# Kernel tuning notes

Hardware: AMD Instinct MI355X
Metric: run time of the kernel (lower is better)

Reference implementation:

```python
import jax, jax.numpy as jnp
import numpy as np

H_DIM = 256
N_HEADS = 8
HALF = H_DIM // 2

def _lin(x, W, b):
    # torch nn.Linear: y = x @ W.T + b
    y = x @ W.T
    return y + b if b is not None else y

def setup_inputs() -> dict:
    key = jax.random.key(0)
    ks = jax.random.split(key, 16)
    s = 0.02
    d = {
        'x': jax.random.normal(ks[0], (16, H_DIM, 32, 32), jnp.float32),
        'q1_w': jax.random.normal(ks[1], (HALF, HALF), jnp.float32) * s,
        'q1_b': jnp.zeros((HALF,), jnp.float32),
        'q2_w': jax.random.normal(ks[2], (HALF, HALF), jnp.float32) * s,
        'q2_b': jnp.zeros((HALF,), jnp.float32),
        'k1_w': jax.random.normal(ks[3], (HALF, HALF), jnp.float32) * s,
        'k1_b': jnp.zeros((HALF,), jnp.float32),
        'k2_w': jax.random.normal(ks[4], (HALF, HALF), jnp.float32) * s,
        'k2_b': jnp.zeros((HALF,), jnp.float32),
        'v1_w': jax.random.normal(ks[5], (HALF, HALF), jnp.float32) * s,
        'v1_b': jnp.zeros((HALF,), jnp.float32),
        'v2_w': jax.random.normal(ks[6], (HALF, HALF), jnp.float32) * s,
        'v2_b': jnp.zeros((HALF,), jnp.float32),
        'proj1_w': jax.random.normal(ks[7], (HALF, HALF), jnp.float32) * s,
        'proj1_b': jnp.zeros((HALF,), jnp.float32),
        'proj2_w': jax.random.normal(ks[8], (HALF, HALF), jnp.float32) * s,
        'proj2_b': jnp.zeros((HALF,), jnp.float32),
        'logit_scale': jnp.log(10.0 * jnp.ones((N_HEADS, 1, 1), jnp.float32)),
        'mlp_w1': jax.random.normal(ks[9], (128, 2), jnp.float32) * s,
        'mlp_b1': jnp.zeros((128,), jnp.float32),
        'mlp_w2': jax.random.normal(ks[10], (N_HEADS, 128), jnp.float32) * s,
    }
    return d

def _rel_pos_index(h, w):
    # static (numpy) relative position index, shape [N, N]
    ch, cw = np.meshgrid(np.arange(h), np.arange(w), indexing='ij')
    coords = np.stack([ch.reshape(-1), cw.reshape(-1)])  # [2, N]
    rel = coords[:, :, None] - coords[:, None, :]         # [2, N, N]
    rel = rel.transpose(1, 2, 0)
    rel[:, :, 0] += h - 1
    rel[:, :, 1] += w - 1
    return rel[:, :, 0] * (2 * w - 1) + rel[:, :, 1]

def _forward(x, q1_w, q1_b, q2_w, q2_b, k1_w, k1_b, k2_w, k2_b,
             v1_w, v1_b, v2_w, v2_b, proj1_w, proj1_b, proj2_w, proj2_b,
             logit_scale, mlp_w1, mlp_b1, mlp_w2):
    b, c, h, w = x.shape
    N = h * w
    nh = N_HEADS
    hd = c // nh
    x3 = jnp.transpose(x, (0, 2, 3, 1)).reshape(b, N, c)
    x0, x1 = x3[..., :c // 2], x3[..., c // 2:]

    def qkv(W0, b0, W1, b1):
        t = jnp.concatenate([x0 + _lin(x0, W0, b0), x1 + _lin(x1, W1, b1)], axis=-1)
        return t.reshape(b, N, nh, hd).transpose(0, 2, 1, 3)  # [b, nh, N, hd]

    q = qkv(q1_w, q1_b, q2_w, q2_b)
    k = qkv(k1_w, k1_b, k2_w, k2_b)
    v = qkv(v1_w, v1_b, v2_w, v2_b)

    eps = 1e-12
    qn = q / jnp.maximum(jnp.linalg.norm(q, axis=-1, keepdims=True), eps)
    kn = k / jnp.maximum(jnp.linalg.norm(k, axis=-1, keepdims=True), eps)
    attn = jnp.einsum('bhnd,bhmd->bhnm', qn, kn)  # cosine similarity
    scale = jnp.exp(jnp.minimum(logit_scale, jnp.log(1.0 / 0.01)))  # [nh,1,1]
    attn = attn * scale[None]

    # continuous relative-position bias (CPB) table via small MLP
    rch = jnp.arange(-(h - 1), h, dtype=jnp.float32) / (h - 1 + 1e-8)
    rcw = jnp.arange(-(w - 1), w, dtype=jnp.float32) / (w - 1 + 1e-8)
    gh, gw = jnp.meshgrid(rch, rcw, indexing='ij')
    tab = jnp.stack([gh, gw], axis=-1) * 3.2               # [2h-1, 2w-1, 2]
    tab = jnp.sign(tab) * (1.0 - jnp.exp(-jnp.abs(tab)))
    tab = jax.nn.relu(_lin(tab, mlp_w1, mlp_b1))
    tab = _lin(tab, mlp_w2, None).reshape(-1, nh)          # [(2h-1)(2w-1), nh]

    idx = jnp.asarray(_rel_pos_index(h, w))                # [N, N]
    bias = tab[idx.reshape(-1)].reshape(N, N, nh).transpose(2, 0, 1)
    bias = 16.0 * jax.nn.sigmoid(bias)
    attn = attn + bias[None]

    attn = jax.nn.softmax(attn, axis=-1)
    out = jnp.einsum('bhnm,bhmd->bhnd', attn, v).transpose(0, 2, 1, 3).reshape(b, N, c)
    o0, o1 = out[..., :c // 2], out[..., c // 2:]
    out = jnp.concatenate([_lin(o0, proj1_w, proj1_b), _lin(o1, proj2_w, proj2_b)], axis=-1)
    return out.reshape(b, h, w, c).transpose(0, 3, 1, 2)

def reference(x, q1_w, q1_b, q2_w, q2_b, k1_w, k1_b, k2_w, k2_b,
              v1_w, v1_b, v2_w, v2_b, proj1_w, proj1_b, proj2_w, proj2_b,
              logit_scale, mlp_w1, mlp_b1, mlp_w2):
    return _forward(x, q1_w, q1_b, q2_w, q2_b, k1_w, k1_b, k2_w, k2_b,
                    v1_w, v1_b, v2_w, v2_b, proj1_w, proj1_b, proj2_w, proj2_b,
                    logit_scale, mlp_w1, mlp_b1, mlp_w2)
```

## Files before the change

kernel.cpp:

```cpp
#include <hip/hip_runtime.h>
#include <cmath>


typedef _Float16 half_t;
typedef __attribute__((ext_vector_type(4))) _Float16 half4;
typedef __attribute__((ext_vector_type(8))) _Float16 half8;
typedef __attribute__((ext_vector_type(4))) float float4v;

static __device__ __forceinline__ float4v mfma16(half8 a, half8 b, float4v c) {
  return __builtin_amdgcn_mfma_f32_16x16x32_f16(a, b, c, 0, 0, 0);
}

struct PtrArr8 { const float* p[8]; };

__global__ __launch_bounds__(256) void prep_w(PtrArr8 wsrc, PtrArr8 bsrc,
                                              half_t* __restrict__ wf,
                                              float* __restrict__ bws) {
  int y = blockIdx.y;
  const float* src = nullptr;
  const float* bs = nullptr;
#pragma unroll
  for (int i = 0; i < 8; i++)
    if (i == y) { src = wsrc.p[i]; bs = bsrc.p[i]; }
  int flat = (blockIdx.x * 256 + threadIdx.x) * 4;
  float4 w = *(const float4*)(src + flat);
  int j = flat >> 7, k = flat & 127;
  if (y < 6) {
    if (k == j)     w.x += 1.0f;
    if (k + 1 == j) w.y += 1.0f;
    if (k + 2 == j) w.z += 1.0f;
    if (k + 3 == j) w.w += 1.0f;
  }
  half4 h;
  h[0] = (half_t)w.x;
  h[1] = (half_t)w.y;
  h[2] = (half_t)w.z;
  h[3] = (half_t)w.w;
  int ng = j >> 4, l = j & 15, ks = k >> 5, quad = (k >> 3) & 3, o8 = k & 7;
  *(half4*)(wf + y * 16384 + ((ng * 4 + ks) * 64 + quad * 16 + l) * 8 + o8) =
      h;
  if (blockIdx.x == 0 && threadIdx.x < 128)
    bws[y * 128 + threadIdx.x] = bs[threadIdx.x];
}

__global__ __launch_bounds__(256) void bias_mlp(const float* __restrict__ w1,
                                                const float* __restrict__ b1,
                                                const float* __restrict__ w2,
                                                const float* __restrict__ ls,
                                                float* __restrict__ tabh2) {
  __shared__ float sw1[256];
  __shared__ float sb1[128];
  __shared__ float sw2[1024];
  int t = threadIdx.x;
  sw1[t] = w1[t];
  if (t < 128) sb1[t] = b1[t];
  for (int i = t; i < 1024; i += 256) sw2[i] = w2[i];
  __syncthreads();
  int p = blockIdx.x * 256 + t;
  if (p >= 3969) return;
  int ph = p / 63, pw = p % 63;
  float t0 = (float)(ph - 31) * (3.2f / 31.0f);
  float t1 = (float)(pw - 31) * (3.2f / 31.0f);
  t0 = copysignf(1.0f - __expf(-fabsf(t0)), t0);
  t1 = copysignf(1.0f - __expf(-fabsf(t1)), t1);
  float acc[8];
#pragma unroll
  for (int hh = 0; hh < 8; hh++) acc[hh] = 0.0f;
  for (int j = 0; j < 128; j++) {
    float hj = fmaxf(0.0f, t0 * sw1[2 * j] + t1 * sw1[2 * j + 1] + sb1[j]);
#pragma unroll
    for (int hh = 0; hh < 8; hh++) acc[hh] += hj * sw2[hh * 128 + j];
  }
  const float L2E = 1.44269504f;
#pragma unroll
  for (int hh = 0; hh < 8; hh++) {
    float scale = __expf(fminf(ls[hh], 4.6051702f));
    float c14 = 14.0f - (scale + 16.0f) * L2E;
    float bias = 16.0f / (1.0f + __expf(-acc[hh]));
    tabh2[hh * 3969 + p] = bias * L2E + c14;
  }
}

__global__ __launch_bounds__(256, 4) void qkv_mfma(
    const float* __restrict__ x, const half_t* __restrict__ wfrag,
    const float* __restrict__ lscale, const float* __restrict__ bws,
    half_t* __restrict__ qf, half_t* __restrict__ kf,
    half_t* __restrict__ vf) {
  __shared__ half_t tbuf[4608];
  int t = threadIdx.x;
  int lane = t & 63, wv = t >> 6, l = lane & 15, quad = lane >> 4;
  int rw = wv & 1, cw = wv >> 1;
  int hf = blockIdx.y;
  int m0 = blockIdx.x * 32;
  int b = m0 >> 10, n0 = m0 & 1023;

  half8 afr[4];
  {
    const float* xb =
        x + ((size_t)b * 256 + hf * 128) * 1024 + n0 + rw * 16 + l;
#pragma unroll
    for (int ks = 0; ks < 4; ks++) {
      half8 a;
#pragma unroll
      for (int j = 0; j < 8; j++)
        a[j] = (half_t)xb[(size_t)(ks * 32 + quad * 8 + j) * 1024];
      afr[ks] = a;
    }
  }

  for (int op = 0; op < 3; op++) {
    int combo = op * 2 + hf;
    const half_t* wfb = wfrag + combo * 16384;
    float4v acc[4];
#pragma unroll
    for (int ngl = 0; ngl < 4; ngl++) {
      int ng = cw * 4 + ngl;
      float4v c = {0.f, 0.f, 0.f, 0.f};
#pragma unroll
      for (int ks = 0; ks < 4; ks++) {
        half8 bfrag =
            *(const half8*)(wfb + ((ng * 4 + ks) * 64 + lane) * 8);
        c = mfma16(afr[ks], bfrag, c);
      }
      acc[ngl] = c;
    }
#pragma unroll
    for (int ngl = 0; ngl < 4; ngl++) {
      float bb = bws[combo * 128 + (cw * 4 + ngl) * 16 + l];
#pragma unroll
      for (int r2 = 0; r2 < 4; r2++) acc[ngl][r2] += bb;
    }
    if (op < 2) {
#pragma unroll
      for (int hgl = 0; hgl < 2; hgl++) {
        float sc = 1.0f;
        if (op == 0)
          sc = __expf(fminf(lscale[hf * 4 + cw * 2 + hgl], 4.6051702f)) *
               1.44269504f;
#pragma unroll
        for (int r2 = 0; r2 < 4; r2++) {
          float ss = acc[2 * hgl][r2] * acc[2 * hgl][r2] +
                     acc[2 * hgl + 1][r2] * acc[2 * hgl + 1][r2];
          ss += __shfl_xor(ss, 1, 64);
          ss += __shfl_xor(ss, 2, 64);
          ss += __shfl_xor(ss, 4, 64);
          ss += __shfl_xor(ss, 8, 64);
          float rn = sc / fmaxf(sqrtf(ss), 1e-12f);
          acc[2 * hgl][r2] *= rn;
          acc[2 * hgl + 1][r2] *= rn;
        }
      }
#pragma unroll
      for (int ngl = 0; ngl < 4; ngl++)
#pragma unroll
        for (int r2 = 0; r2 < 4; r2++)
          tbuf[(rw * 16 + quad * 4 + r2) * 136 + (cw * 4 + ngl) * 16 + l] =
              (half_t)acc[ngl][r2];
      __syncthreads();
      half_t* dst = (op == 0) ? qf : kf;
#pragma unroll
      for (int i = 0; i < 2; i++) {
        int idx = t + 256 * i;
        int row = idx >> 4, colc = (idx & 15) * 8;
        half8 vv = *(const half8*)(tbuf + row * 136 + colc);
        int head = hf * 4 + (colc >> 5), d = colc & 31;
        *(half8*)(dst + (((size_t)b * 8 + head) * 1024 + n0 + row) * 32 + d) =
            vv;
      }
      __syncthreads();
    } else {
#pragma unroll
      for (int ngl = 0; ngl < 4; ngl++) {
        int col = (cw * 4 + ngl) * 16 + l;
        half4 hv;
#pragma unroll
        for (int r2 = 0; r2 < 4; r2++) hv[r2] = (half_t)acc[ngl][r2];
        *(half4*)(tbuf + col * 36 + rw * 16 + quad * 4) = hv;
      }
      __syncthreads();
#pragma unroll
      for (int i = 0; i < 8; i++) {
        int idx = t + 256 * i;
        int col = idx >> 4, rp = idx & 15;
        unsigned int val = *(const unsigned int*)(tbuf + col * 36 + rp * 2);
        int head = hf * 4 + (col >> 5);
        int d = col & 31;
        *(unsigned int*)((char*)vf +
                         (((((size_t)b * 8 + head) * 32 + d) * 1024) + n0 +
                          rp * 2) * 2) = val;
      }
    }
  }
}

__global__ __launch_bounds__(256) void attn_mfma(
    const half_t* __restrict__ qf, const half_t* __restrict__ kf,
    const half_t* __restrict__ vf, const float* __restrict__ tabh2,
    half_t* __restrict__ ao) {
  __shared__ float sb2[35 * 63];
  __shared__ half_t pa[4 * 16 * 80];

  int id = blockIdx.x;
  int qo = id >> 7;
  int bh = id & 127;
  int h = bh & 7, b = bh >> 3;
  int t = threadIdx.x;
  int lane = t & 63, wv = t >> 6, l = lane & 15, quad = lane >> 4;
  size_t bhs = (size_t)b * 8 + h;
  const half_t* kbase = kf + bhs * 1024 * 32;
  const half_t* vbase = vf + bhs * 32 * 1024;

  for (int i = t; i < 2205; i += 256)
    sb2[i] = tabh2[h * 3969 + qo * 252 + i];

  int row0 = qo * 128 + wv * 32;
  half8 qfr[2];
#pragma unroll
  for (int s = 0; s < 2; s++)
    qfr[s] = *(const half8*)(qf + (bhs * 1024 + row0 + s * 16 + l) * 32 +
                             quad * 8);

  float4v o0[2], o1[2];
  float run_l[2];
#pragma unroll
  for (int s = 0; s < 2; s++) {
    o0[s] = (float4v){0.f, 0.f, 0.f, 0.f};
    o1[s] = (float4v){0.f, 0.f, 0.f, 0.f};
    run_l[s] = 0.0f;
  }
  half_t* paw = pa + wv * 16 * 80;
  __syncthreads();

#pragma unroll 2
  for (int kt = 0; kt < 16; kt++) {
    half8 kfr[4], v0fr[2], v1fr[2];
#pragma unroll
    for (int nt = 0; nt < 4; nt++)
      kfr[nt] =
          *(const half8*)(kbase + (kt * 64 + nt * 16 + l) * 32 + quad * 8);
#pragma unroll
    for (int ks = 0; ks < 2; ks++) {
      v0fr[ks] = *(const half8*)(vbase + l * 1024 + kt * 64 + ks * 32 +
                                 quad * 8);
      v1fr[ks] = *(const half8*)(vbase + (16 + l) * 1024 + kt * 64 + ks * 32 +
                                 quad * 8);
    }
#pragma unroll
    for (int s = 0; s < 2; s++) {
      float4v sres[4];
#pragma unroll
      for (int nt = 0; nt < 4; nt++) {
        int base = (wv - 2 * kt - (nt >> 1) + 31) * 63 + s * 16 + l + 31 -
                   (nt & 1) * 16 - quad * 4;
        float4v c;
        c[0] = sb2[base];
        c[1] = sb2[base - 1];
        c[2] = sb2[base - 2];
        c[3] = sb2[base - 3];
        sres[nt] = mfma16(kfr[nt], qfr[s], c);
      }
#pragma unroll
      for (int nt = 0; nt < 4; nt++) {
        half4 ph;
#pragma unroll
        for (int r2 = 0; r2 < 4; r2++) {
          float p = exp2f(sres[nt][r2]);
          run_l[s] += p;
          ph[r2] = (half_t)p;
        }
        *(half4*)(paw + l * 80 + nt * 16 + quad * 4) = ph;
      }
#pragma unroll
      for (int ks = 0; ks < 2; ks++) {
        half8 pfr = *(const half8*)(paw + l * 80 + ks * 32 + quad * 8);
        o0[s] = mfma16(pfr, v0fr[ks], o0[s]);
        o1[s] = mfma16(pfr, v1fr[ks], o1[s]);
      }
    }
  }

#pragma unroll
  for (int s = 0; s < 2; s++) {
    float rl = run_l[s];
    rl += __shfl_xor(rl, 16, 64);
    rl += __shfl_xor(rl, 32, 64);
    float rli = 1.0f / rl;
#pragma unroll
    for (int r2 = 0; r2 < 4; r2++) {
      float linv = __shfl(rli, 20 * quad + r2, 64);
      size_t rowaddr =
          ((size_t)b * 1024 + row0 + s * 16 + quad * 4 + r2) * 256 + h * 32;
      ao[rowaddr + l] = (half_t)(o0[s][r2] * linv);
      ao[rowaddr + 16 + l] = (half_t)(o1[s][r2] * linv);
    }
  }
}

__global__ __launch_bounds__(256, 4) void proj_mfma(
    const half_t* __restrict__ ao, const half_t* __restrict__ wfrag,
    const float* __restrict__ bws, float* __restrict__ out) {
  __shared__ float yt[128 * 36];
  int t = threadIdx.x;
  int lane = t & 63, wv = t >> 6, l = lane & 15, quad = lane >> 4;
  int rw = wv & 1, cw = wv >> 1;
  int hf = blockIdx.y;
  int m0 = blockIdx.x * 32;
  int b = m0 >> 10, n0 = m0 & 1023;

  half8 afr[4];
  const half_t* ab =
      ao + ((size_t)m0 + rw * 16 + l) * 256 + hf * 128 + quad * 8;
#pragma unroll
  for (int ks = 0; ks < 4; ks++) afr[ks] = *(const half8*)(ab + ks * 32);

  const half_t* wfb = wfrag + (6 + hf) * 16384;
#pragma unroll
  for (int ngl = 0; ngl < 4; ngl++) {
    int ng = cw * 4 + ngl;
    float4v c = {0.f, 0.f, 0.f, 0.f};
#pragma unroll
    for (int ks = 0; ks < 4; ks++) {
      half8 bfrag = *(const half8*)(wfb + ((ng * 4 + ks) * 64 + lane) * 8);
      c = mfma16(afr[ks], bfrag, c);
    }
    float bb = bws[(6 + hf) * 128 + ng * 16 + l];
#pragma unroll
    for (int r2 = 0; r2 < 4; r2++) c[r2] += bb;
    *(float4v*)(yt + (ng * 16 + l) * 36 + rw * 16 + quad * 4) = c;
  }
  __syncthreads();
#pragma unroll
  for (int i = 0; i < 4; i++) {
    int idx = t + 256 * i;
    int col = idx >> 3, rg = idx & 7;
    float4v vv = *(const float4v*)(yt + col * 36 + rg * 4);
    *(float4v*)(out + ((size_t)b * 256 + hf * 128 + col) * 1024 + n0 +
                rg * 4) = vv;
  }
}

extern "C" void kernel_launch(void* const* d_in, const int* in_sizes, int n_in,
                              void* d_out, int out_size, void* d_ws,
                              size_t ws_size, hipStream_t stream) {
  (void)in_sizes; (void)n_in; (void)out_size; (void)ws_size;
  const float* x = (const float*)d_in[0];

  half_t* ws = (half_t*)d_ws;
  half_t* qfp = ws;
  half_t* kfp = ws + 4194304;
  half_t* vfp = ws + 8388608;
  half_t* aop = ws + 12582912;
  half_t* wfp = ws + 16777216;
  float* tabh2 = (float*)((char*)d_ws + 33816576);
  float* bws = (float*)((char*)d_ws + 33943584);

  PtrArr8 wsrc, bsrc;
  const int widx[8] = {1, 3, 5, 7, 9, 11, 13, 15};
  for (int i = 0; i < 8; i++) {
    wsrc.p[i] = (const float*)d_in[widx[i]];
    bsrc.p[i] = (const float*)d_in[widx[i] + 1];
  }

  prep_w<<<dim3(16, 8), 256, 0, stream>>>(wsrc, bsrc, wfp, bws);
  bias_mlp<<<16, 256, 0, stream>>>((const float*)d_in[18],
                                   (const float*)d_in[19],
                                   (const float*)d_in[20],
                                   (const float*)d_in[17], tabh2);
  qkv_mfma<<<dim3(512, 2), 256, 0, stream>>>(x, wfp, (const float*)d_in[17],
                                             bws, qfp, kfp, vfp);
  attn_mfma<<<1024, 256, 0, stream>>>(qfp, kfp, vfp, tabh2, aop);
  proj_mfma<<<dim3(512, 2), 256, 0, stream>>>(aop, wfp, bws, (float*)d_out);
}
```

Baseline: 188.1 us.

## Split attention into 64-row query tiles, fuse prep kernels, batch QKV stores

```diff
diff --git a/kernel.cpp b/kernel.cpp
--- a/kernel.cpp
+++ b/kernel.cpp
@@ -13,50 +13,47 @@
 
 struct PtrArr8 { const float* p[8]; };
 
-__global__ __launch_bounds__(256) void prep_w(PtrArr8 wsrc, PtrArr8 bsrc,
-                                              half_t* __restrict__ wf,
-                                              float* __restrict__ bws) {
-  int y = blockIdx.y;
-  const float* src = nullptr;
-  const float* bs = nullptr;
-#pragma unroll
-  for (int i = 0; i < 8; i++)
-    if (i == y) { src = wsrc.p[i]; bs = bsrc.p[i]; }
-  int flat = (blockIdx.x * 256 + threadIdx.x) * 4;
-  float4 w = *(const float4*)(src + flat);
-  int j = flat >> 7, k = flat & 127;
-  if (y < 6) {
-    if (k == j)     w.x += 1.0f;
-    if (k + 1 == j) w.y += 1.0f;
-    if (k + 2 == j) w.z += 1.0f;
-    if (k + 3 == j) w.w += 1.0f;
-  }
-  half4 h;
-  h[0] = (half_t)w.x;
-  h[1] = (half_t)w.y;
-  h[2] = (half_t)w.z;
-  h[3] = (half_t)w.w;
-  int ng = j >> 4, l = j & 15, ks = k >> 5, quad = (k >> 3) & 3, o8 = k & 7;
-  *(half4*)(wf + y * 16384 + ((ng * 4 + ks) * 64 + quad * 16 + l) * 8 + o8) =
-      h;
-  if (blockIdx.x == 0 && threadIdx.x < 128)
-    bws[y * 128 + threadIdx.x] = bs[threadIdx.x];
-}
-
-__global__ __launch_bounds__(256) void bias_mlp(const float* __restrict__ w1,
-                                                const float* __restrict__ b1,
-                                                const float* __restrict__ w2,
-                                                const float* __restrict__ ls,
-                                                float* __restrict__ tabh2) {
+__global__ __launch_bounds__(256) void prep_fused(
+    PtrArr8 wsrc, PtrArr8 bsrc, const float* __restrict__ w1,
+    const float* __restrict__ b1, const float* __restrict__ w2,
+    const float* __restrict__ ls, half_t* __restrict__ wf,
+    float* __restrict__ bws, float* __restrict__ tabh2) {
+  int t = threadIdx.x;
+  if (blockIdx.x < 128) {
+    int y = blockIdx.x & 7, xb = blockIdx.x >> 3;
+    const float* src = nullptr;
+    const float* bs = nullptr;
+#pragma unroll
+    for (int i = 0; i < 8; i++)
+      if (i == y) { src = wsrc.p[i]; bs = bsrc.p[i]; }
+    int flat = (xb * 256 + t) * 4;
+    float4 w = *(const float4*)(src + flat);
+    int j = flat >> 7, k = flat & 127;
+    if (y < 6) {
+      if (k == j)     w.x += 1.0f;
+      if (k + 1 == j) w.y += 1.0f;
+      if (k + 2 == j) w.z += 1.0f;
+      if (k + 3 == j) w.w += 1.0f;
+    }
+    half4 h;
+    h[0] = (half_t)w.x;
+    h[1] = (half_t)w.y;
+    h[2] = (half_t)w.z;
+    h[3] = (half_t)w.w;
+    int ng = j >> 4, l = j & 15, ks = k >> 5, quad = (k >> 3) & 3, o8 = k & 7;
+    *(half4*)(wf + y * 16384 + ((ng * 4 + ks) * 64 + quad * 16 + l) * 8 +
+              o8) = h;
+    if (xb == 0 && t < 128) bws[y * 128 + t] = bs[t];
+    return;
+  }
   __shared__ float sw1[256];
   __shared__ float sb1[128];
   __shared__ float sw2[1024];
-  int t = threadIdx.x;
   sw1[t] = w1[t];
   if (t < 128) sb1[t] = b1[t];
   for (int i = t; i < 1024; i += 256) sw2[i] = w2[i];
   __syncthreads();
-  int p = blockIdx.x * 256 + t;
+  int p = (blockIdx.x - 128) * 256 + t;
   if (p >= 3969) return;
   int ph = p / 63, pw = p % 63;
   float t0 = (float)(ph - 31) * (3.2f / 31.0f);
@@ -86,7 +83,9 @@
     const float* __restrict__ lscale, const float* __restrict__ bws,
     half_t* __restrict__ qf, half_t* __restrict__ kf,
     half_t* __restrict__ vf) {
-  __shared__ half_t tbuf[4608];
+  __shared__ half_t qbuf[32 * 136];
+  __shared__ half_t kbuf[32 * 136];
+  __shared__ half_t vbuf[128 * 36];
   int t = threadIdx.x;
   int lane = t & 63, wv = t >> 6, l = lane & 15, quad = lane >> 4;
   int rw = wv & 1, cw = wv >> 1;
@@ -108,6 +107,7 @@
     }
   }
 
+#pragma unroll
   for (int op = 0; op < 3; op++) {
     int combo = op * 2 + hf;
     const half_t* wfb = wfrag + combo * 16384;
@@ -118,8 +118,7 @@
       float4v c = {0.f, 0.f, 0.f, 0.f};
 #pragma unroll
       for (int ks = 0; ks < 4; ks++) {
-        half8 bfrag =
-            *(const half8*)(wfb + ((ng * 4 + ks) * 64 + lane) * 8);
+        half8 bfrag = *(const half8*)(wfb + ((ng * 4 + ks) * 64 + lane) * 8);
         c = mfma16(afr[ks], bfrag, c);
       }
       acc[ngl] = c;
@@ -150,24 +149,13 @@
           acc[2 * hgl + 1][r2] *= rn;
         }
       }
+      half_t* tb = (op == 0) ? qbuf : kbuf;
 #pragma unroll
       for (int ngl = 0; ngl < 4; ngl++)
 #pragma unroll
         for (int r2 = 0; r2 < 4; r2++)
-          tbuf[(rw * 16 + quad * 4 + r2) * 136 + (cw * 4 + ngl) * 16 + l] =
+          tb[(rw * 16 + quad * 4 + r2) * 136 + (cw * 4 + ngl) * 16 + l] =
               (half_t)acc[ngl][r2];
-      __syncthreads();
-      half_t* dst = (op == 0) ? qf : kf;
-#pragma unroll
-      for (int i = 0; i < 2; i++) {
-        int idx = t + 256 * i;
-        int row = idx >> 4, colc = (idx & 15) * 8;
-        half8 vv = *(const half8*)(tbuf + row * 136 + colc);
-        int head = hf * 4 + (colc >> 5), d = colc & 31;
-        *(half8*)(dst + (((size_t)b * 8 + head) * 1024 + n0 + row) * 32 + d) =
-            vv;
-      }
-      __syncthreads();
     } else {
 #pragma unroll
       for (int ngl = 0; ngl < 4; ngl++) {
@@ -175,33 +163,42 @@
         half4 hv;
 #pragma unroll
         for (int r2 = 0; r2 < 4; r2++) hv[r2] = (half_t)acc[ngl][r2];
-        *(half4*)(tbuf + col * 36 + rw * 16 + quad * 4) = hv;
+        *(half4*)(vbuf + col * 36 + rw * 16 + quad * 4) = hv;
       }
-      __syncthreads();
-#pragma unroll
-      for (int i = 0; i < 8; i++) {
-        int idx = t + 256 * i;
-        int col = idx >> 4, rp = idx & 15;
-        unsigned int val = *(const unsigned int*)(tbuf + col * 36 + rp * 2);
-        int head = hf * 4 + (col >> 5);
-        int d = col & 31;
-        *(unsigned int*)((char*)vf +
-                         (((((size_t)b * 8 + head) * 32 + d) * 1024) + n0 +
-                          rp * 2) * 2) = val;
-      }
-    }
-  }
-}
-
-__global__ __launch_bounds__(256) void attn_mfma(
+    }
+  }
+  __syncthreads();
+
+#pragma unroll
+  for (int i = 0; i < 2; i++) {
+    int idx = t + 256 * i;
+    int row = idx >> 4, colc = (idx & 15) * 8;
+    int head = hf * 4 + (colc >> 5), d = colc & 31;
+    size_t off = (((size_t)b * 8 + head) * 1024 + n0 + row) * 32 + d;
+    *(half8*)(qf + off) = *(const half8*)(qbuf + row * 136 + colc);
+    *(half8*)(kf + off) = *(const half8*)(kbuf + row * 136 + colc);
+  }
+#pragma unroll
+  for (int i = 0; i < 8; i++) {
+    int idx = t + 256 * i;
+    int col = idx >> 4, rp = idx & 15;
+    unsigned int val = *(const unsigned int*)(vbuf + col * 36 + rp * 2);
+    int head = hf * 4 + (col >> 5);
+    int d = col & 31;
+    *(unsigned int*)((char*)vf + (((((size_t)b * 8 + head) * 32 + d) * 1024) +
+                                  n0 + rp * 2) * 2) = val;
+  }
+}
+
+__global__ __launch_bounds__(256, 6) void attn_mfma(
     const half_t* __restrict__ qf, const half_t* __restrict__ kf,
     const half_t* __restrict__ vf, const float* __restrict__ tabh2,
     half_t* __restrict__ ao) {
-  __shared__ float sb2[35 * 63];
+  __shared__ float sb2[33 * 63];
   __shared__ half_t pa[4 * 16 * 80];
 
   int id = blockIdx.x;
-  int qo = id >> 7;
+  int qt = id >> 7;
   int bh = id & 127;
   int h = bh & 7, b = bh >> 3;
   int t = threadIdx.x;
@@ -210,24 +207,17 @@
   const half_t* kbase = kf + bhs * 1024 * 32;
   const half_t* vbase = vf + bhs * 32 * 1024;
 
-  for (int i = t; i < 2205; i += 256)
-    sb2[i] = tabh2[h * 3969 + qo * 252 + i];
-
-  int row0 = qo * 128 + wv * 32;
-  half8 qfr[2];
-#pragma unroll
-  for (int s = 0; s < 2; s++)
-    qfr[s] = *(const half8*)(qf + (bhs * 1024 + row0 + s * 16 + l) * 32 +
-                             quad * 8);
-
-  float4v o0[2], o1[2];
-  float run_l[2];
-#pragma unroll
-  for (int s = 0; s < 2; s++) {
-    o0[s] = (float4v){0.f, 0.f, 0.f, 0.f};
-    o1[s] = (float4v){0.f, 0.f, 0.f, 0.f};
-    run_l[s] = 0.0f;
-  }
+  for (int i = t; i < 2079; i += 256)
+    sb2[i] = tabh2[h * 3969 + qt * 126 + i];
+
+  int row0 = qt * 64 + wv * 16;
+  int iw0 = (wv & 1) * 16;
+  int whalf = wv >> 1;
+
+  half8 qfr = *(const half8*)(qf + (bhs * 1024 + row0 + l) * 32 + quad * 8);
+
+  float4v o0 = {0.f, 0.f, 0.f, 0.f}, o1 = {0.f, 0.f, 0.f, 0.f};
+  float run_l = 0.0f;
   half_t* paw = pa + wv * 16 * 80;
   __syncthreads();
 
@@ -240,59 +230,53 @@
           *(const half8*)(kbase + (kt * 64 + nt * 16 + l) * 32 + quad * 8);
 #pragma unroll
     for (int ks = 0; ks < 2; ks++) {
-      v0fr[ks] = *(const half8*)(vbase + l * 1024 + kt * 64 + ks * 32 +
-                                 quad * 8);
+      v0fr[ks] =
+          *(const half8*)(vbase + l * 1024 + kt * 64 + ks * 32 + quad * 8);
       v1fr[ks] = *(const half8*)(vbase + (16 + l) * 1024 + kt * 64 + ks * 32 +
                                  quad * 8);
     }
-#pragma unroll
-    for (int s = 0; s < 2; s++) {
-      float4v sres[4];
-#pragma unroll
-      for (int nt = 0; nt < 4; nt++) {
-        int base = (wv - 2 * kt - (nt >> 1) + 31) * 63 + s * 16 + l + 31 -
-                   (nt & 1) * 16 - quad * 4;
-        float4v c;
-        c[0] = sb2[base];
-        c[1] = sb2[base - 1];
-        c[2] = sb2[base - 2];
-        c[3] = sb2[base - 3];
-        sres[nt] = mfma16(kfr[nt], qfr[s], c);
+    float4v sres[4];
+#pragma unroll
+    for (int nt = 0; nt < 4; nt++) {
+      int base = (whalf - 2 * kt - (nt >> 1) + 31) * 63 + iw0 + l + 31 -
+                 (nt & 1) * 16 - quad * 4;
+      float4v c;
+      c[0] = sb2[base];
+      c[1] = sb2[base - 1];
+      c[2] = sb2[base - 2];
+      c[3] = sb2[base - 3];
+      sres[nt] = mfma16(kfr[nt], qfr, c);
+    }
+#pragma unroll
+    for (int nt = 0; nt < 4; nt++) {
+      half4 ph;
+#pragma unroll
+      for (int r2 = 0; r2 < 4; r2++) {
+        float p = exp2f(sres[nt][r2]);
+        run_l += p;
+        ph[r2] = (half_t)p;
       }
-#pragma unroll
-      for (int nt = 0; nt < 4; nt++) {
-        half4 ph;
-#pragma unroll
-        for (int r2 = 0; r2 < 4; r2++) {
-          float p = exp2f(sres[nt][r2]);
-          run_l[s] += p;
-          ph[r2] = (half_t)p;
-        }
-        *(half4*)(paw + l * 80 + nt * 16 + quad * 4) = ph;
-      }
-#pragma unroll
-      for (int ks = 0; ks < 2; ks++) {
-        half8 pfr = *(const half8*)(paw + l * 80 + ks * 32 + quad * 8);
-        o0[s] = mfma16(pfr, v0fr[ks], o0[s]);
-        o1[s] = mfma16(pfr, v1fr[ks], o1[s]);
-      }
-    }
-  }
-
-#pragma unroll
-  for (int s = 0; s < 2; s++) {
-    float rl = run_l[s];
-    rl += __shfl_xor(rl, 16, 64);
-    rl += __shfl_xor(rl, 32, 64);
-    float rli = 1.0f / rl;
-#pragma unroll
-    for (int r2 = 0; r2 < 4; r2++) {
-      float linv = __shfl(rli, 20 * quad + r2, 64);
-      size_t rowaddr =
-          ((size_t)b * 1024 + row0 + s * 16 + quad * 4 + r2) * 256 + h * 32;
-      ao[rowaddr + l] = (half_t)(o0[s][r2] * linv);
-      ao[rowaddr + 16 + l] = (half_t)(o1[s][r2] * linv);
-    }
+      *(half4*)(paw + l * 80 + nt * 16 + quad * 4) = ph;
+    }
+#pragma unroll
+    for (int ks = 0; ks < 2; ks++) {
+      half8 pfr = *(const half8*)(paw + l * 80 + ks * 32 + quad * 8);
+      o0 = mfma16(pfr, v0fr[ks], o0);
+      o1 = mfma16(pfr, v1fr[ks], o1);
+    }
+  }
+
+  run_l += __shfl_xor(run_l, 16, 64);
+  run_l += __shfl_xor(run_l, 32, 64);
+  float rli = 1.0f / run_l;
+
+#pragma unroll
+  for (int r2 = 0; r2 < 4; r2++) {
+    float linv = __shfl(rli, 20 * quad + r2, 64);
+    size_t rowaddr =
+        ((size_t)b * 1024 + row0 + quad * 4 + r2) * 256 + h * 32;
+    ao[rowaddr + l] = (half_t)(o0[r2] * linv);
+    ao[rowaddr + 16 + l] = (half_t)(o1[r2] * linv);
   }
 }
 
@@ -361,13 +345,11 @@
     bsrc.p[i] = (const float*)d_in[widx[i] + 1];
   }
 
-  prep_w<<<dim3(16, 8), 256, 0, stream>>>(wsrc, bsrc, wfp, bws);
-  bias_mlp<<<16, 256, 0, stream>>>((const float*)d_in[18],
-                                   (const float*)d_in[19],
-                                   (const float*)d_in[20],
-                                   (const float*)d_in[17], tabh2);
+  prep_fused<<<144, 256, 0, stream>>>(
+      wsrc, bsrc, (const float*)d_in[18], (const float*)d_in[19],
+      (const float*)d_in[20], (const float*)d_in[17], wfp, bws, tabh2);
   qkv_mfma<<<dim3(512, 2), 256, 0, stream>>>(x, wfp, (const float*)d_in[17],
                                              bws, qfp, kfp, vfp);
-  attn_mfma<<<1024, 256, 0, stream>>>(qfp, kfp, vfp, tabh2, aop);
+  attn_mfma<<<2048, 256, 0, stream>>>(qfp, kfp, vfp, tabh2, aop);
   proj_mfma<<<dim3(512, 2), 256, 0, stream>>>(aop, wfp, bws, (float*)d_out);
 }
```

Result: slower. 245.5 us (+30.5%).
